# Optimization experiments

Hardware: AMD Instinct MI355X
Metric: run time of the kernel (lower is better)

Reference implementation:

```python
import jax, jax.numpy as jnp
import numpy as np

B, DAYS, N, E = 2, 8, 10000, 80000
C_IN, C_OUT, H = 32, 32, 4
NEG_SLOPE = 0.2


def setup_inputs() -> dict:
    key = jax.random.key(0)
    ks = jax.random.split(key, 7)
    x = jax.random.randint(ks[0], (B, DAYS, N), 0, N)
    adjacency = jax.random.randint(ks[1], (2, E), 0, N)
    embedding = jax.random.normal(ks[2], (N, C_IN), dtype=jnp.float32)
    # GATConv linear: in_channels -> heads*out_channels
    W = jax.random.normal(ks[3], (C_IN, H * C_OUT), dtype=jnp.float32) / np.sqrt(C_IN)
    att_src = jax.random.normal(ks[4], (H, C_OUT), dtype=jnp.float32) / np.sqrt(C_OUT)
    att_dst = jax.random.normal(ks[5], (H, C_OUT), dtype=jnp.float32) / np.sqrt(C_OUT)
    bias = jnp.zeros((H * C_OUT,), dtype=jnp.float32)
    return {"x": x, "adjacency": adjacency, "embedding": embedding,
            "W": W, "att_src": att_src, "att_dst": att_dst, "bias": bias}


def _gat_forward(feat, src, dst, W, att_src, att_dst, bias):
    # feat: [G, N, C_IN]; same edge list shared across the G graphs
    G = feat.shape[0]
    xh = (feat @ W).reshape(G, N, H, C_OUT)              # [G,N,H,C]
    a_src = jnp.einsum('gnhc,hc->gnh', xh, att_src)       # [G,N,H]
    a_dst = jnp.einsum('gnhc,hc->gnh', xh, att_dst)
    alpha = a_src[:, src] + a_dst[:, dst]                 # [G,Et,H]
    alpha = jnp.where(alpha >= 0, alpha, NEG_SLOPE * alpha)

    def per_graph(al, msgs):
        # segment softmax over incoming edges of each dst node
        m = jax.ops.segment_max(al, dst, num_segments=N)  # [N,H]
        e = jnp.exp(al - m[dst])                          # [Et,H]
        s = jax.ops.segment_sum(e, dst, num_segments=N)
        w = e / (s[dst] + 1e-16)
        out = jax.ops.segment_sum(w[..., None] * msgs, dst, num_segments=N)
        return out                                        # [N,H,C]

    out = jax.vmap(per_graph)(alpha, xh[:, src])          # [G,N,H,C]
    return out.reshape(G, N, H * C_OUT) + bias


def reference(x, adjacency, embedding, W, att_src, att_dst, bias):
    Bd, Dd = x.shape[0], x.shape[1]
    feat = embedding[x].reshape(-1, N, C_IN)              # [G,N,C_IN]
    # GATConv default add_self_loops=True
    loops = jnp.arange(N, dtype=adjacency.dtype)
    src = jnp.concatenate([adjacency[0], loops])
    dst = jnp.concatenate([adjacency[1], loops])
    out = _gat_forward(feat, src, dst, W, att_src, att_dst, bias)
    return out.reshape(Bd, Dd, -1)
```

## Files before the change

### kernel.cpp

```cpp
#include <hip/hip_runtime.h>
#include <hip/hip_bf16.h>
#include <math.h>

#define C_IN 32
#define H 4
#define C_OUT 32
#define HC (H * C_OUT)
#define NEG_SLOPE 0.2f
#define CSR_STRIDE 64

typedef float v2f __attribute__((ext_vector_type(2)));

#define RPB 16
__global__ __launch_bounds__(256) void build_kernel(
        const int* __restrict__ adj, int E, int N,
        int* __restrict__ deg, int* __restrict__ csr,
        const float* __restrict__ emb, const float* __restrict__ W,
        const float* __restrict__ att_src, const float* __restrict__ att_dst,
        __hip_bfloat16* __restrict__ T, float* __restrict__ ta_src,
        float* __restrict__ ta_dst, int tblocks) {
    if ((int)blockIdx.x >= tblocks) {
        int e = (blockIdx.x - tblocks) * 256 + threadIdx.x;
        int Et = E + N;
        if (e < Et) {
            int s = (e < E) ? adj[e] : (e - E);
            int d = (e < E) ? adj[E + e] : (e - E);
            int pos = atomicAdd(&deg[d], 1);
            if (pos < CSR_STRIDE) csr[(d << 6) + pos] = s;
        }
        return;
    }
    int t = threadIdx.x;
    int sub = t >> 7;
    int tc = t & 127;
    int h = tc >> 5, c = tc & 31;
    int base = blockIdx.x * RPB;
    int nmax = (N - base < RPB) ? (N - base) : RPB;

    float wcol[C_IN];
#pragma unroll
    for (int k = 0; k < C_IN; k++) wcol[k] = W[k * HC + tc];
    float as = att_src[h * C_OUT + c];
    float adw = att_dst[h * C_OUT + c];

    for (int it = sub; it < nmax; it += 2) {
        int r = __builtin_amdgcn_readfirstlane(base + it);
        const float* ep = emb + (size_t)r * C_IN;
        float acc = 0.f;
#pragma unroll
        for (int k = 0; k < C_IN; k++) acc += ep[k] * wcol[k];
        T[(size_t)r * HC + tc] = __float2bfloat16(acc);
        float ps = acc * as, pd = acc * adw;
#pragma unroll
        for (int o = 16; o; o >>= 1) {
            ps += __shfl_xor(ps, o, 32);
            pd += __shfl_xor(pd, o, 32);
        }
        if (c == 0) {
            ta_src[r * H + h] = ps;
            ta_dst[r * H + h] = pd;
        }
    }
}

__global__ __launch_bounds__(256) void agg_kernel(
        const int* __restrict__ deg, const int* __restrict__ csr,
        const int* __restrict__ x, const unsigned int* __restrict__ Tu,
        const float* __restrict__ ta_src, const float* __restrict__ ta_dst,
        const float* __restrict__ bias, float* __restrict__ out, int N, int G) {
    __shared__ float w_lds[CSR_STRIDE][16][4];
    __shared__ int   xs8_lds[16][65];
    __shared__ float ds_lds[16][4];

    int t = threadIdx.x;
    int n = blockIdx.x;
    int dg = deg[n];
    if (dg > CSR_STRIDE) dg = CSR_STRIDE;
    const int* cb = csr + (n << 6);

    {
        int g = t >> 4;
        int es = (t >> 2) & 3;
        int h = t & 3;
        int xgn = x[(size_t)g * N + n];
        float adv = ta_dst[xgn * H + h];
        float dpart = 0.f;
        for (int c0 = 0; c0 < dg; c0 += 4) {
            int e = c0 + es;
            if (e < dg) {
                int s = cb[e];
                int xs = x[(size_t)g * N + s];
                float a = ta_src[xs * H + h] + adv;
                a = fmaxf(a, NEG_SLOPE * a);
                float w = __expf(a);
                w_lds[e][g][h] = w;
                dpart += w;
                if (h == 0) xs8_lds[g][e] = xs << 8;
            }
        }
        dpart += __shfl_xor(dpart, 4, 64);
        dpart += __shfl_xor(dpart, 8, 64);
        if (es == 0) ds_lds[g][h] = dpart;
    }
    __syncthreads();

    int wid = t >> 6;
    int lane = t & 63;
    int lg = lane >> 4;
    int li = lane & 15;
    int gj = wid * 4 + lg;
    int hh = li >> 2;
    int li16 = li << 4;

    v2f a0 = {0.f, 0.f}, a1 = {0.f, 0.f}, a2 = {0.f, 0.f}, a3 = {0.f, 0.f};

#pragma unroll 2
    for (int e = 0; e < dg; e++) {
        int off = xs8_lds[gj][e] + li16;
        float w = w_lds[e][gj][hh];
        uint4 u = *(const uint4*)((const char*)Tu + off);
        a0.x += w * __uint_as_float(u.x << 16);
        a0.y += w * __uint_as_float(u.x & 0xffff0000u);
        a1.x += w * __uint_as_float(u.y << 16);
        a1.y += w * __uint_as_float(u.y & 0xffff0000u);
        a2.x += w * __uint_as_float(u.z << 16);
        a2.y += w * __uint_as_float(u.z & 0xffff0000u);
        a3.x += w * __uint_as_float(u.w << 16);
        a3.y += w * __uint_as_float(u.w & 0xffff0000u);
    }

    float inv = __builtin_amdgcn_rcpf(ds_lds[gj][hh] + 1e-16f);
    const float4* bp = (const float4*)(bias + li * 8);
    float4 b0 = bp[0], b1 = bp[1];
    float4 o0 = {a0.x * inv + b0.x, a0.y * inv + b0.y,
                 a1.x * inv + b0.z, a1.y * inv + b0.w};
    float4 o1 = {a2.x * inv + b1.x, a2.y * inv + b1.y,
                 a3.x * inv + b1.z, a3.y * inv + b1.w};
    float* op = out + (size_t)gj * N * HC + (size_t)n * HC + li * 8;
    *(float4*)op = o0;
    *(float4*)(op + 4) = o1;
}

extern "C" void kernel_launch(void* const* d_in, const int* in_sizes, int n_in,
                              void* d_out, int out_size, void* d_ws, size_t ws_size,
                              hipStream_t stream) {
    const int*   x       = (const int*)d_in[0];
    const int*   adj     = (const int*)d_in[1];
    const float* emb     = (const float*)d_in[2];
    const float* W       = (const float*)d_in[3];
    const float* att_src = (const float*)d_in[4];
    const float* att_dst = (const float*)d_in[5];
    const float* bias    = (const float*)d_in[6];
    float* out = (float*)d_out;

    const int N  = in_sizes[2] / C_IN;
    const int GN = in_sizes[0];
    const int G  = GN / N;
    const int E  = in_sizes[1] / 2;
    const int Et = E + N;

    char* ws = (char*)d_ws;
    size_t o = 0;
    auto carve = [&](size_t bytes) -> void* {
        void* p = ws + o;
        o = (o + bytes + 255) & ~(size_t)255;
        return p;
    };
    __hip_bfloat16* T = (__hip_bfloat16*)carve((size_t)N * HC * sizeof(__hip_bfloat16));
    float* ta_src  = (float*)carve((size_t)N * H * sizeof(float));
    float* ta_dst  = (float*)carve((size_t)N * H * sizeof(float));
    int*   deg     = (int*)carve((size_t)N * sizeof(int));
    int*   csr     = (int*)carve((size_t)N * CSR_STRIDE * sizeof(int));

    hipMemsetAsync(deg, 0, (size_t)N * sizeof(int), stream);

    int tblocks = (N + RPB - 1) / RPB;
    int fblocks = (Et + 255) / 256;
    build_kernel<<<tblocks + fblocks, 256, 0, stream>>>(
        adj, E, N, deg, csr, emb, W, att_src, att_dst, T, ta_src, ta_dst, tblocks);

    agg_kernel<<<N, 256, 0, stream>>>(deg, csr, x,
                                      (const unsigned int*)T, ta_src, ta_dst,
                                      bias, out, N, G);
}
```

Before: 150.2 us.

## Fold attention vectors into W and stage embedding rows in LDS

Precomputes W·att_src and W·att_dst per block so attention logits come from a small 32x4 dot product on the embedding row, dropping the per-row shuffle reductions. Embedding rows are staged in shared memory, and each block now handles 4 rows instead of 16, giving more blocks. The trade-off is that every block recomputes the folded attention matrices and reloads the W columns, so the fixed per-block overhead grows as rows per block shrink.

Result: slower. 163.7 us (+9.0%).

```diff
diff --git a/kernel.cpp b/kernel.cpp
--- a/kernel.cpp
+++ b/kernel.cpp
@@ -8,10 +8,10 @@
 #define HC (H * C_OUT)
 #define NEG_SLOPE 0.2f
 #define CSR_STRIDE 64
+#define TROWS 4
 
 typedef float v2f __attribute__((ext_vector_type(2)));
 
-#define RPB 16
 __global__ __launch_bounds__(256) void build_kernel(
         const int* __restrict__ adj, int E, int N,
         int* __restrict__ deg, int* __restrict__ csr,
@@ -30,35 +30,67 @@
         }
         return;
     }
+    __shared__ float se[TROWS][C_IN];
+    __shared__ float sws[C_IN][H];
+    __shared__ float swd[C_IN][H];
+
     int t = threadIdx.x;
-    int sub = t >> 7;
+    int base = blockIdx.x * TROWS;
+    int nmax = N - base;
+    if (nmax > TROWS) nmax = TROWS;
+
+    if (t < TROWS * (C_IN / 4)) {
+        int r = t >> 3;
+        int k4 = t & 7;
+        if (r < nmax)
+            ((float4*)se[r])[k4] =
+                ((const float4*)(emb + (size_t)(base + r) * C_IN))[k4];
+    }
+    {
+        int kk = (t & 127) >> 2;
+        int h = t & 3;
+        const float* av = (t < 128) ? att_src : att_dst;
+        const float* wr = W + kk * HC + h * C_OUT;
+        float s = 0.f;
+#pragma unroll
+        for (int c = 0; c < C_OUT; c++) s += wr[c] * av[h * C_OUT + c];
+        if (t < 128) sws[kk][h] = s;
+        else         swd[kk][h] = s;
+    }
+    __syncthreads();
+
     int tc = t & 127;
-    int h = tc >> 5, c = tc & 31;
-    int base = blockIdx.x * RPB;
-    int nmax = (N - base < RPB) ? (N - base) : RPB;
-
+    int rs = t >> 7;
     float wcol[C_IN];
 #pragma unroll
     for (int k = 0; k < C_IN; k++) wcol[k] = W[k * HC + tc];
-    float as = att_src[h * C_OUT + c];
-    float adw = att_dst[h * C_OUT + c];
-
-    for (int it = sub; it < nmax; it += 2) {
-        int r = __builtin_amdgcn_readfirstlane(base + it);
-        const float* ep = emb + (size_t)r * C_IN;
-        float acc = 0.f;
-#pragma unroll
-        for (int k = 0; k < C_IN; k++) acc += ep[k] * wcol[k];
-        T[(size_t)r * HC + tc] = __float2bfloat16(acc);
-        float ps = acc * as, pd = acc * adw;
-#pragma unroll
-        for (int o = 16; o; o >>= 1) {
-            ps += __shfl_xor(ps, o, 32);
-            pd += __shfl_xor(pd, o, 32);
-        }
-        if (c == 0) {
-            ta_src[r * H + h] = ps;
-            ta_dst[r * H + h] = pd;
+
+#pragma unroll
+    for (int rr = 0; rr < 2; rr++) {
+        int r = rs + rr * 2;
+        if (r < nmax) {
+            float acc = 0.f;
+#pragma unroll
+            for (int k = 0; k < C_IN; k++) acc += se[r][k] * wcol[k];
+            T[(size_t)(base + r) * HC + tc] = __float2bfloat16(acc);
+        }
+    }
+
+    if (t < TROWS * 2 * H) {
+        int r = t >> 3;
+        int sel = (t >> 2) & 1;
+        int h = t & 3;
+        if (r < nmax) {
+            float s = 0.f;
+            if (sel) {
+#pragma unroll
+                for (int k = 0; k < C_IN; k++) s += se[r][k] * swd[k][h];
+                ta_dst[(base + r) * H + h] = s;
+            } else {
+#pragma unroll
+                for (int k = 0; k < C_IN; k++) s += se[r][k] * sws[k][h];
+                ta_src[(base + r) * H + h] = s;
+            }
         }
     }
 }
@@ -174,7 +206,7 @@
 
     hipMemsetAsync(deg, 0, (size_t)N * sizeof(int), stream);
 
-    int tblocks = (N + RPB - 1) / RPB;
+    int tblocks = (N + TROWS - 1) / TROWS;
     int fblocks = (Et + 255) / 256;
     build_kernel<<<tblocks + fblocks, 256, 0, stream>>>(
         adj, E, N, deg, csr, emb, W, att_src, att_dst, T, ta_src, ta_dst, tblocks);
```
